# Optimization experiments

Hardware: AMD Instinct MI355X
Metric: run time of the kernel (lower is better)

The kernel has to match this reference:

```python
import jax, jax.numpy as jnp
import numpy as np


def setup_inputs() -> dict:
    key = jax.random.key(0)
    k1, k2 = jax.random.split(key)
    h = jax.random.normal(k1, (8, 16, 64, 512), dtype=jnp.float32)
    M = jax.random.normal(k2, (20000, 512), dtype=jnp.float32)
    return {"h": h, "M": M}


def reference(h, M):
    # h: [B, T, X, R], M: [K, R]
    B, T, X, R = h.shape
    hf = h.reshape(-1, R)                      # [N, R]
    att = jax.nn.softmax(hf @ M.T, axis=1)     # [N, K], unscaled dot-product
    out = att @ M                              # [N, R]
    return out.reshape(B, T, X, R)
```

## Files before the change

kernel.cpp:

```cpp
#include <hip/hip_runtime.h>
#include <stdint.h>

#define NQ 8192
#define NK 20000
#define RD 512
#define NT 157
#define TS0 79

typedef float f32x4 __attribute__((ext_vector_type(4)));
typedef short s16x8 __attribute__((ext_vector_type(8)));

__device__ __forceinline__ unsigned short bf16_rn(float x) {
    uint32_t u = __float_as_uint(x);
    return (unsigned short)((u + 0x7FFFu + ((u >> 16) & 1)) >> 16);
}

__device__ __forceinline__ void lds_barrier() {
    asm volatile("s_waitcnt lgkmcnt(0)\n\ts_barrier" ::: "memory");
}

__global__ void preconv_kernel(const float* __restrict__ M,
                               unsigned short* __restrict__ Mhi,
                               unsigned short* __restrict__ Mlo,
                               unsigned short* __restrict__ MT) {
    __shared__ float tilef[64 * 65];
    const int k0 = blockIdx.x * 64, r0 = blockIdx.y * 64;
    const int t = threadIdx.x;
#pragma unroll
    for (int i = 0; i < 16; i++) {
        int e = t + i * 256;
        int kr = e >> 6, cc = e & 63;
        int key = k0 + kr;
        if (key < NK) {
            float x = M[(size_t)key * RD + r0 + cc];
            uint32_t u = __float_as_uint(x);
            Mhi[(size_t)key * RD + r0 + cc] = (unsigned short)(u >> 16);
            Mlo[(size_t)key * RD + r0 + cc] = bf16_rn(x - __uint_as_float(u & 0xFFFF0000u));
            tilef[cc * 65 + kr] = x;
        }
    }
    __syncthreads();
#pragma unroll
    for (int i = 0; i < 16; i++) {
        int e = t + i * 256;
        int rr = e >> 6, kk = e & 63;
        int key = k0 + kk;
        if (key < NK) MT[(size_t)(r0 + rr) * NK + key] = bf16_rn(tilef[rr * 65 + kk]);
    }
}

__global__ __launch_bounds__(256, 2) void flash6_kernel(
        const float* __restrict__ h,
        const unsigned short* __restrict__ Mhi,
        const unsigned short* __restrict__ Mlo,
        const unsigned short* __restrict__ MT,
        float* __restrict__ out,
        float* __restrict__ Opart,
        float* __restrict__ mpart,
        float* __restrict__ lpart,
        int nsplit) {
    __shared__ unsigned short qbuf[32768];
    __shared__ unsigned short pbuf[8 * 512];
    __shared__ float smaxb[4 * 2 * 16];
    __shared__ float ssumb[4 * 2 * 16];

    const int tid = threadIdx.x;
    const int ch = tid >> 6, l = tid & 63;
    const int l15 = l & 15, q4 = l >> 4;
    const int kq = (l15 >> 3) & 1, jj = l15 & 7;

    int qb, split;
    if (nsplit == 2) { split = blockIdx.x & 1; qb = blockIdx.x >> 1; }
    else             { split = 0;              qb = blockIdx.x; }
    const int koff = (split == 0) ? 0 : TS0 * 128;
    const int ntl  = (nsplit == 2) ? ((split == 0) ? TS0 : (NT - TS0)) : NT;
    const int total_ks = ntl * 16;
    const int qbase = qb * 32;

    const size_t base_w = (size_t)(ch * 32 + l15) * RD + q4 * 8;
    auto kaddr = [&](int g, int cb) -> size_t {
        if (g >= total_ks) g = total_ks - 1;
        int t2 = g >> 4, s2 = g & 15;
        return (size_t)(koff + t2 * 128) * RD + (size_t)s2 * 32 + base_w + (size_t)cb * (16 * RD);
    };

    s16x8 kh[2][4], kl[2][4];
#pragma unroll
    for (int i = 0; i < 4; i++) {
        size_t a0 = kaddr(i, 0), a1 = kaddr(i, 1);
        kh[0][i] = *(const s16x8*)(Mhi + a0);
        kl[0][i] = *(const s16x8*)(Mlo + a0);
        kh[1][i] = *(const s16x8*)(Mhi + a1);
        kl[1][i] = *(const s16x8*)(Mlo + a1);
    }

#pragma unroll
    for (int i = 0; i < 8; i++) {
        int g = tid + i * 256;
        int row = g >> 6, s = (g >> 2) & 15, qg = g & 3;
        int strip = row >> 4, lrow = row & 15;
        const float* src = h + (size_t)(qbase + row) * RD + s * 32 + qg * 8;
        f32x4 a = *(const f32x4*)src;
        f32x4 b = *(const f32x4*)(src + 4);
        s16x8 hi8, lo8;
#pragma unroll
        for (int j = 0; j < 8; j++) {
            float x = (j < 4) ? a[j] : b[j - 4];
            uint32_t u = __float_as_uint(x);
            hi8[j] = (short)(u >> 16);
            lo8[j] = (short)bf16_rn(x - __uint_as_float(u & 0xFFFF0000u));
        }
        int off = ((strip * 16 + s) * 512 + (qg * 16 + lrow) * 8);
        *(s16x8*)&qbuf[off] = hi8;
        *(s16x8*)&qbuf[16384 + off] = lo8;
    }
    lds_barrier();

    f32x4 O[2][8];
#pragma unroll
    for (int st = 0; st < 2; st++)
#pragma unroll
        for (int ct = 0; ct < 8; ct++) O[st][ct] = 0.f;
    f32x4 m_run[2], l_run[2];
    m_run[0] = -3e38f; m_run[1] = -3e38f; l_run[0] = 0.f; l_run[1] = 0.f;

    for (int tile = 0; tile < ntl; tile++) {
        f32x4 C[2][2];
        C[0][0] = 0.f; C[0][1] = 0.f; C[1][0] = 0.f; C[1][1] = 0.f;
#pragma unroll
        for (int s = 0; s < 16; s++) {
            const int sl = s & 3;
            s16x8 kh0 = kh[0][sl], kl0 = kl[0][sl];
            s16x8 kh1 = kh[1][sl], kl1 = kl[1][sl];
            {
                int g = tile * 16 + s + 4;
                size_t a0 = kaddr(g, 0), a1 = kaddr(g, 1);
                kh[0][sl] = *(const s16x8*)(Mhi + a0);
                kl[0][sl] = *(const s16x8*)(Mlo + a0);
                kh[1][sl] = *(const s16x8*)(Mhi + a1);
                kl[1][sl] = *(const s16x8*)(Mlo + a1);
            }
#pragma unroll
            for (int st = 0; st < 2; st++) {
                s16x8 qh = *(const s16x8*)&qbuf[(st * 16 + s) * 512 + l * 8];
                s16x8 ql = *(const s16x8*)&qbuf[16384 + (st * 16 + s) * 512 + l * 8];
                C[st][0] = __builtin_amdgcn_mfma_f32_16x16x32_bf16(qh, kh0, C[st][0], 0, 0, 0);
                C[st][1] = __builtin_amdgcn_mfma_f32_16x16x32_bf16(qh, kh1, C[st][1], 0, 0, 0);
                C[st][0] = __builtin_amdgcn_mfma_f32_16x16x32_bf16(ql, kh0, C[st][0], 0, 0, 0);
                C[st][1] = __builtin_amdgcn_mfma_f32_16x16x32_bf16(ql, kh1, C[st][1], 0, 0, 0);
                C[st][0] = __builtin_amdgcn_mfma_f32_16x16x32_bf16(qh, kl0, C[st][0], 0, 0, 0);
                C[st][1] = __builtin_amdgcn_mfma_f32_16x16x32_bf16(qh, kl1, C[st][1], 0, 0, 0);
            }
        }
        if (tile == ntl - 1) {
#pragma unroll
            for (int cb = 0; cb < 2; cb++) {
                int kg = koff + tile * 128 + ch * 32 + cb * 16 + l15;
                if (kg >= NK) { C[0][cb] = -3e38f; C[1][cb] = -3e38f; }
            }
        }

        const unsigned short* mtp = MT + (size_t)(ch * 128 + l15) * NK + koff + tile * 128 + q4 * 8;
        s16x8 bt[2][4];
#pragma unroll
        for (int sk = 0; sk < 4; sk++) {
            bt[0][sk] = *(const s16x8*)(mtp + sk * 32);
            bt[1][sk] = *(const s16x8*)(mtp + (size_t)16 * NK + sk * 32);
        }

        f32x4 mx[2];
#pragma unroll
        for (int st = 0; st < 2; st++)
#pragma unroll
            for (int v = 0; v < 4; v++) mx[st][v] = fmaxf(C[st][0][v], C[st][1][v]);
#pragma unroll
        for (int d = 1; d < 16; d <<= 1) {
#pragma unroll
            for (int st = 0; st < 2; st++)
#pragma unroll
                for (int v = 0; v < 4; v++) mx[st][v] = fmaxf(mx[st][v], __shfl_xor(mx[st][v], d, 16));
        }
        if (l15 == 0) {
            *(f32x4*)&smaxb[(ch * 2 + 0) * 16 + q4 * 4] = mx[0];
            *(f32x4*)&smaxb[(ch * 2 + 1) * 16 + q4 * 4] = mx[1];
        }
        lds_barrier();
        f32x4 mnew[2]; mnew[0] = m_run[0]; mnew[1] = m_run[1];
#pragma unroll
        for (int cc = 0; cc < 4; cc++) {
#pragma unroll
            for (int st = 0; st < 2; st++) {
                f32x4 tv = *(const f32x4*)&smaxb[(cc * 2 + st) * 16 + q4 * 4];
#pragma unroll
                for (int v = 0; v < 4; v++) mnew[st][v] = fmaxf(mnew[st][v], tv[v]);
            }
        }
        f32x4 alpha[2];
#pragma unroll
        for (int st = 0; st < 2; st++)
#pragma unroll
            for (int v = 0; v < 4; v++) {
                alpha[st][v] = __expf(m_run[st][v] - mnew[st][v]);
                m_run[st][v] = mnew[st][v];
            }
        f32x4 ps[2]; ps[0] = 0.f; ps[1] = 0.f;
#pragma unroll
        for (int st = 0; st < 2; st++) {
#pragma unroll
            for (int cb = 0; cb < 2; cb++) {
#pragma unroll
                for (int v = 0; v < 4; v++) {
                    float p = __expf(C[st][cb][v] - mnew[st][v]);
                    ps[st][v] += p;
                    pbuf[(ch * 2 + st) * 512 + ((cb * 2 + kq) * 16 + q4 * 4 + v) * 8 + jj] = bf16_rn(p);
                }
            }
        }
#pragma unroll
        for (int d = 1; d < 16; d <<= 1) {
#pragma unroll
            for (int st = 0; st < 2; st++)
#pragma unroll
                for (int v = 0; v < 4; v++) ps[st][v] += __shfl_xor(ps[st][v], d, 16);
        }
        if (l15 == 0) {
            *(f32x4*)&ssumb[(ch * 2 + 0) * 16 + q4 * 4] = ps[0];
            *(f32x4*)&ssumb[(ch * 2 + 1) * 16 + q4 * 4] = ps[1];
        }
        lds_barrier();
        f32x4 ts[2]; ts[0] = 0.f; ts[1] = 0.f;
#pragma unroll
        for (int cc = 0; cc < 4; cc++) {
            ts[0] += *(const f32x4*)&ssumb[(cc * 2 + 0) * 16 + q4 * 4];
            ts[1] += *(const f32x4*)&ssumb[(cc * 2 + 1) * 16 + q4 * 4];
        }
#pragma unroll
        for (int st = 0; st < 2; st++)
#pragma unroll
            for (int v = 0; v < 4; v++) l_run[st][v] = l_run[st][v] * alpha[st][v] + ts[st][v];
#pragma unroll
        for (int st = 0; st < 2; st++)
#pragma unroll
            for (int ct = 0; ct < 8; ct++)
#pragma unroll
                for (int v = 0; v < 4; v++) O[st][ct][v] *= alpha[st][v];
        s16x8 pa[2][4];
#pragma unroll
        for (int st = 0; st < 2; st++)
#pragma unroll
            for (int sk = 0; sk < 4; sk++)
                pa[st][sk] = *(const s16x8*)&pbuf[((sk * 2 + st) * 512) + l * 8];

#pragma unroll
        for (int ct = 0; ct < 8; ct++) {
            s16x8 b0 = bt[ct & 1][0], b1 = bt[ct & 1][1], b2 = bt[ct & 1][2], b3 = bt[ct & 1][3];
            if (ct < 6) {
#pragma unroll
                for (int sk = 0; sk < 4; sk++)
                    bt[ct & 1][sk] = *(const s16x8*)(mtp + (size_t)(ct + 2) * 16 * NK + sk * 32);
            }
            O[0][ct] = __builtin_amdgcn_mfma_f32_16x16x32_bf16(pa[0][0], b0, O[0][ct], 0, 0, 0);
            O[1][ct] = __builtin_amdgcn_mfma_f32_16x16x32_bf16(pa[1][0], b0, O[1][ct], 0, 0, 0);
            O[0][ct] = __builtin_amdgcn_mfma_f32_16x16x32_bf16(pa[0][1], b1, O[0][ct], 0, 0, 0);
            O[1][ct] = __builtin_amdgcn_mfma_f32_16x16x32_bf16(pa[1][1], b1, O[1][ct], 0, 0, 0);
            O[0][ct] = __builtin_amdgcn_mfma_f32_16x16x32_bf16(pa[0][2], b2, O[0][ct], 0, 0, 0);
            O[1][ct] = __builtin_amdgcn_mfma_f32_16x16x32_bf16(pa[1][2], b2, O[1][ct], 0, 0, 0);
            O[0][ct] = __builtin_amdgcn_mfma_f32_16x16x32_bf16(pa[0][3], b3, O[0][ct], 0, 0, 0);
            O[1][ct] = __builtin_amdgcn_mfma_f32_16x16x32_bf16(pa[1][3], b3, O[1][ct], 0, 0, 0);
        }
        lds_barrier();
    }

    if (nsplit == 2) {
        float* Od = Opart + (size_t)split * NQ * RD;
#pragma unroll
        for (int st = 0; st < 2; st++)
#pragma unroll
            for (int ct = 0; ct < 8; ct++)
#pragma unroll
                for (int v = 0; v < 4; v++)
                    Od[(size_t)(qbase + st * 16 + q4 * 4 + v) * RD + ch * 128 + ct * 16 + l15] =
                        O[st][ct][v];
        if (ch == 0 && l15 == 0) {
#pragma unroll
            for (int st = 0; st < 2; st++)
#pragma unroll
                for (int v = 0; v < 4; v++) {
                    mpart[split * NQ + qbase + st * 16 + q4 * 4 + v] = m_run[st][v];
                    lpart[split * NQ + qbase + st * 16 + q4 * 4 + v] = l_run[st][v];
                }
        }
    } else {
#pragma unroll
        for (int st = 0; st < 2; st++)
#pragma unroll
            for (int ct = 0; ct < 8; ct++)
#pragma unroll
                for (int v = 0; v < 4; v++)
                    out[(size_t)(qbase + st * 16 + q4 * 4 + v) * RD + ch * 128 + ct * 16 + l15] =
                        O[st][ct][v] / l_run[st][v];
    }
}

__global__ __launch_bounds__(256) void combine_kernel(const float* __restrict__ Opart,
                                                      const float* __restrict__ mpart,
                                                      const float* __restrict__ lpart,
                                                      float* __restrict__ out) {
    const int t = threadIdx.x;
    const int row = blockIdx.x * 2 + (t >> 7);
    const int d = (t & 127) * 4;
    float m0 = mpart[row], m1 = mpart[NQ + row];
    float l0 = lpart[row], l1 = lpart[NQ + row];
    float m = fmaxf(m0, m1);
    float w0 = __expf(m0 - m), w1 = __expf(m1 - m);
    float inv = 1.f / (w0 * l0 + w1 * l1);
    f32x4 o0 = *(const f32x4*)&Opart[(size_t)row * RD + d];
    f32x4 o1 = *(const f32x4*)&Opart[(size_t)NQ * RD + (size_t)row * RD + d];
    f32x4 r;
#pragma unroll
    for (int v = 0; v < 4; v++) r[v] = (o0[v] * w0 + o1[v] * w1) * inv;
    *(f32x4*)&out[(size_t)row * RD + d] = r;
}

__global__ __launch_bounds__(256) void naive_kernel(const float* __restrict__ h,
                                                    const float* __restrict__ M,
                                                    float* __restrict__ out) {
    __shared__ float hs[16 * 520];
    __shared__ float ms[8 * 520];
    __shared__ float sdot[2][128];
    __shared__ float sm[16], sl[16], sal[16], sp[16][8];
    const int t = threadIdx.x;
    const int qbase = blockIdx.x * 16;
#pragma unroll
    for (int i = 0; i < 32; i++) {
        int e = t + i * 256;
        int row = e >> 9, col = e & 511;
        hs[row * 520 + col] = h[(size_t)(qbase + row) * RD + col];
    }
    if (t < 16) { sm[t] = -3e38f; sl[t] = 0.f; }
    float Oacc[32];
#pragma unroll
    for (int i = 0; i < 32; i++) Oacc[i] = 0.f;
    const int q = t >> 4;
    const int eb = (t & 15) * 32;

    for (int k0 = 0; k0 < NK; k0 += 8) {
        __syncthreads();
#pragma unroll
        for (int i = 0; i < 16; i++) {
            int e = t + i * 256;
            if (e < 4096) {
                int kk = e >> 9, col = e & 511;
                ms[kk * 520 + col] = M[(size_t)(k0 + kk) * RD + col];
            }
        }
        __syncthreads();
        {
            int pair = t & 127, half = t >> 7;
            int qq = pair & 15, kk = pair >> 4;
            const float* hp = &hs[qq * 520 + half * 256];
            const float* mp = &ms[kk * 520 + half * 256];
            float acc = 0.f;
#pragma unroll 8
            for (int e = 0; e < 256; e++) acc += hp[e] * mp[e];
            sdot[half][pair] = acc;
        }
        __syncthreads();
        if (t < 16) {
            int qq = t;
            float s8[8];
#pragma unroll
            for (int kk = 0; kk < 8; kk++) s8[kk] = sdot[0][qq + 16 * kk] + sdot[1][qq + 16 * kk];
            float mn = sm[qq];
#pragma unroll
            for (int kk = 0; kk < 8; kk++) mn = fmaxf(mn, s8[kk]);
            float al = __expf(sm[qq] - mn);
            float addl = 0.f;
#pragma unroll
            for (int kk = 0; kk < 8; kk++) { float p = __expf(s8[kk] - mn); sp[qq][kk] = p; addl += p; }
            sm[qq] = mn; sl[qq] = sl[qq] * al + addl; sal[qq] = al;
        }
        __syncthreads();
        {
            float al = sal[q];
#pragma unroll
            for (int i = 0; i < 32; i++) Oacc[i] *= al;
#pragma unroll
            for (int kk = 0; kk < 8; kk++) {
                float p = sp[q][kk];
                const float* mp = &ms[kk * 520 + eb];
#pragma unroll
                for (int i = 0; i < 32; i++) Oacc[i] += p * mp[i];
            }
        }
    }
    __syncthreads();
    float inv = 1.f / sl[q];
#pragma unroll
    for (int i = 0; i < 32; i++) out[(size_t)(qbase + q) * RD + eb + i] = Oacc[i] * inv;
}

extern "C" void kernel_launch(void* const* d_in, const int* in_sizes, int n_in,
                              void* d_out, int out_size, void* d_ws, size_t ws_size,
                              hipStream_t stream) {
    const float* h = (const float*)d_in[0];
    const float* M = (const float*)d_in[1];
    float* out = (float*)d_out;
    const size_t seg = (size_t)NK * RD;
    const size_t base_bytes = (seg * 3ull + 8192ull) * 2ull;
    const size_t opart_bytes = 2ull * NQ * RD * 4ull;
    const size_t stat_bytes = 2ull * 2ull * NQ * 4ull;
    const size_t need_split = base_bytes + opart_bytes + stat_bytes;

    if (ws_size >= base_bytes) {
        unsigned short* Mhi = (unsigned short*)d_ws;
        unsigned short* Mlo = Mhi + seg;
        unsigned short* MT  = Mlo + seg;
        float* Opart = (float*)((char*)d_ws + base_bytes);
        float* mpart = Opart + 2ull * NQ * RD;
        float* lpart = mpart + 2ull * NQ;
        preconv_kernel<<<dim3(313, 8), 256, 0, stream>>>(M, Mhi, Mlo, MT);
        if (ws_size >= need_split) {
            flash6_kernel<<<512, 256, 0, stream>>>(h, Mhi, Mlo, MT, out, Opart, mpart, lpart, 2);
            combine_kernel<<<NQ / 2, 256, 0, stream>>>(Opart, mpart, lpart, out);
        } else {
            flash6_kernel<<<256, 256, 0, stream>>>(h, Mhi, Mlo, MT, out, Opart, mpart, lpart, 1);
        }
    } else {
        naive_kernel<<<512, 256, 0, stream>>>(h, M, out);
    }
}
```

Baseline: 1.593 ms.

## Software-pipeline QK^T of next tile with softmax and PV of previous tile

Restructures the main loop so the QK^T MFMA steps for tile i are split into chunks and interleaved around the barriers of the softmax/PV phase for tile i-1. The last tile is handled in an epilogue after the loop, and the trailing per-iteration barrier is dropped. The aim is to hide barrier waits, exp work and LDS latency behind matrix work. Keeping two score tiles live raises register pressure, which could cause spills.

```diff
diff --git a/kernel.cpp b/kernel.cpp
--- a/kernel.cpp
+++ b/kernel.cpp
@@ -49,7 +49,32 @@
     }
 }
 
-__global__ __launch_bounds__(256, 2) void flash6_kernel(
+#define S_STEP(ii, s_) do {                                                                        \
+        const int sl_ = (s_) & 3;                                                                  \
+        s16x8 kh0_ = kh[0][sl_], kl0_ = kl[0][sl_];                                                \
+        s16x8 kh1_ = kh[1][sl_], kl1_ = kl[1][sl_];                                                \
+        {                                                                                          \
+            int g_ = (ii) * 16 + (s_) + 4;                                                         \
+            size_t a0_ = kaddr(g_, 0), a1_ = kaddr(g_, 1);                                         \
+            kh[0][sl_] = *(const s16x8*)(Mhi + a0_);                                               \
+            kl[0][sl_] = *(const s16x8*)(Mlo + a0_);                                               \
+            kh[1][sl_] = *(const s16x8*)(Mhi + a1_);                                               \
+            kl[1][sl_] = *(const s16x8*)(Mlo + a1_);                                               \
+        }                                                                                          \
+        _Pragma("unroll")                                                                          \
+        for (int st_ = 0; st_ < 2; st_++) {                                                        \
+            s16x8 qh_ = *(const s16x8*)&qbuf[(st_ * 16 + (s_)) * 512 + l * 8];                     \
+            s16x8 ql_ = *(const s16x8*)&qbuf[16384 + (st_ * 16 + (s_)) * 512 + l * 8];             \
+            Cc[st_][0] = __builtin_amdgcn_mfma_f32_16x16x32_bf16(qh_, kh0_, Cc[st_][0], 0, 0, 0);  \
+            Cc[st_][1] = __builtin_amdgcn_mfma_f32_16x16x32_bf16(qh_, kh1_, Cc[st_][1], 0, 0, 0);  \
+            Cc[st_][0] = __builtin_amdgcn_mfma_f32_16x16x32_bf16(ql_, kh0_, Cc[st_][0], 0, 0, 0);  \
+            Cc[st_][1] = __builtin_amdgcn_mfma_f32_16x16x32_bf16(ql_, kh1_, Cc[st_][1], 0, 0, 0);  \
+            Cc[st_][0] = __builtin_amdgcn_mfma_f32_16x16x32_bf16(qh_, kl0_, Cc[st_][0], 0, 0, 0);  \
+            Cc[st_][1] = __builtin_amdgcn_mfma_f32_16x16x32_bf16(qh_, kl1_, Cc[st_][1], 0, 0, 0);  \
+        }                                                                                          \
+    } while (0)
+
+__global__ __launch_bounds__(256, 2) void flash7_kernel(
         const float* __restrict__ h,
         const unsigned short* __restrict__ Mhi,
         const unsigned short* __restrict__ Mlo,
@@ -124,55 +149,33 @@
     f32x4 m_run[2], l_run[2];
     m_run[0] = -3e38f; m_run[1] = -3e38f; l_run[0] = 0.f; l_run[1] = 0.f;
 
-    for (int tile = 0; tile < ntl; tile++) {
-        f32x4 C[2][2];
-        C[0][0] = 0.f; C[0][1] = 0.f; C[1][0] = 0.f; C[1][1] = 0.f;
-#pragma unroll
-        for (int s = 0; s < 16; s++) {
-            const int sl = s & 3;
-            s16x8 kh0 = kh[0][sl], kl0 = kl[0][sl];
-            s16x8 kh1 = kh[1][sl], kl1 = kl[1][sl];
-            {
-                int g = tile * 16 + s + 4;
-                size_t a0 = kaddr(g, 0), a1 = kaddr(g, 1);
-                kh[0][sl] = *(const s16x8*)(Mhi + a0);
-                kl[0][sl] = *(const s16x8*)(Mlo + a0);
-                kh[1][sl] = *(const s16x8*)(Mhi + a1);
-                kl[1][sl] = *(const s16x8*)(Mlo + a1);
-            }
-#pragma unroll
-            for (int st = 0; st < 2; st++) {
-                s16x8 qh = *(const s16x8*)&qbuf[(st * 16 + s) * 512 + l * 8];
-                s16x8 ql = *(const s16x8*)&qbuf[16384 + (st * 16 + s) * 512 + l * 8];
-                C[st][0] = __builtin_amdgcn_mfma_f32_16x16x32_bf16(qh, kh0, C[st][0], 0, 0, 0);
-                C[st][1] = __builtin_amdgcn_mfma_f32_16x16x32_bf16(qh, kh1, C[st][1], 0, 0, 0);
-                C[st][0] = __builtin_amdgcn_mfma_f32_16x16x32_bf16(ql, kh0, C[st][0], 0, 0, 0);
-                C[st][1] = __builtin_amdgcn_mfma_f32_16x16x32_bf16(ql, kh1, C[st][1], 0, 0, 0);
-                C[st][0] = __builtin_amdgcn_mfma_f32_16x16x32_bf16(qh, kl0, C[st][0], 0, 0, 0);
-                C[st][1] = __builtin_amdgcn_mfma_f32_16x16x32_bf16(qh, kl1, C[st][1], 0, 0, 0);
-            }
-        }
-        if (tile == ntl - 1) {
-#pragma unroll
-            for (int cb = 0; cb < 2; cb++) {
-                int kg = koff + tile * 128 + ch * 32 + cb * 16 + l15;
-                if (kg >= NK) { C[0][cb] = -3e38f; C[1][cb] = -3e38f; }
-            }
-        }
-
-        const unsigned short* mtp = MT + (size_t)(ch * 128 + l15) * NK + koff + tile * 128 + q4 * 8;
+    f32x4 Cc[2][2];
+    Cc[0][0] = 0.f; Cc[0][1] = 0.f; Cc[1][0] = 0.f; Cc[1][1] = 0.f;
+#pragma unroll
+    for (int s = 0; s < 16; s++) S_STEP(0, s);
+
+    for (int i = 1; i < ntl; i++) {
+        const int prv = i - 1;
+
+        f32x4 Cp[2][2];
+#pragma unroll
+        for (int st = 0; st < 2; st++) {
+            Cp[st][0] = Cc[st][0]; Cp[st][1] = Cc[st][1];
+            Cc[st][0] = 0.f;       Cc[st][1] = 0.f;
+        }
+
+        const unsigned short* mtp = MT + (size_t)(ch * 128 + l15) * NK + koff + prv * 128 + q4 * 8;
         s16x8 bt[2][4];
 #pragma unroll
         for (int sk = 0; sk < 4; sk++) {
             bt[0][sk] = *(const s16x8*)(mtp + sk * 32);
             bt[1][sk] = *(const s16x8*)(mtp + (size_t)16 * NK + sk * 32);
         }
-
         f32x4 mx[2];
 #pragma unroll
         for (int st = 0; st < 2; st++)
 #pragma unroll
-            for (int v = 0; v < 4; v++) mx[st][v] = fmaxf(C[st][0][v], C[st][1][v]);
+            for (int v = 0; v < 4; v++) mx[st][v] = fmaxf(Cp[st][0][v], Cp[st][1][v]);
 #pragma unroll
         for (int d = 1; d < 16; d <<= 1) {
 #pragma unroll
@@ -184,7 +187,10 @@
             *(f32x4*)&smaxb[(ch * 2 + 0) * 16 + q4 * 4] = mx[0];
             *(f32x4*)&smaxb[(ch * 2 + 1) * 16 + q4 * 4] = mx[1];
         }
+#pragma unroll
+        for (int s = 0; s < 5; s++) S_STEP(i, s);
         lds_barrier();
+
         f32x4 mnew[2]; mnew[0] = m_run[0]; mnew[1] = m_run[1];
 #pragma unroll
         for (int cc = 0; cc < 4; cc++) {
@@ -210,7 +216,7 @@
             for (int cb = 0; cb < 2; cb++) {
 #pragma unroll
                 for (int v = 0; v < 4; v++) {
-                    float p = __expf(C[st][cb][v] - mnew[st][v]);
+                    float p = __expf(Cp[st][cb][v] - mnew[st][v]);
                     ps[st][v] += p;
                     pbuf[(ch * 2 + st) * 512 + ((cb * 2 + kq) * 16 + q4 * 4 + v) * 8 + jj] = bf16_rn(p);
                 }
@@ -227,7 +233,10 @@
             *(f32x4*)&ssumb[(ch * 2 + 0) * 16 + q4 * 4] = ps[0];
             *(f32x4*)&ssumb[(ch * 2 + 1) * 16 + q4 * 4] = ps[1];
         }
+#pragma unroll
+        for (int s = 5; s < 11; s++) S_STEP(i, s);
         lds_barrier();
+
         f32x4 ts[2]; ts[0] = 0.f; ts[1] = 0.f;
 #pragma unroll
         for (int cc = 0; cc < 4; cc++) {
@@ -250,7 +259,8 @@
 #pragma unroll
             for (int sk = 0; sk < 4; sk++)
                 pa[st][sk] = *(const s16x8*)&pbuf[((sk * 2 + st) * 512) + l * 8];
-
+#pragma unroll
+        for (int s = 11; s < 16; s++) S_STEP(i, s);
 #pragma unroll
         for (int ct = 0; ct < 8; ct++) {
             s16x8 b0 = bt[ct & 1][0], b1 = bt[ct & 1][1], b2 = bt[ct & 1][2], b3 = bt[ct & 1][3];
@@ -268,7 +278,121 @@
             O[0][ct] = __builtin_amdgcn_mfma_f32_16x16x32_bf16(pa[0][3], b3, O[0][ct], 0, 0, 0);
             O[1][ct] = __builtin_amdgcn_mfma_f32_16x16x32_bf16(pa[1][3], b3, O[1][ct], 0, 0, 0);
         }
+    }
+
+    {
+        const int prv = ntl - 1;
+#pragma unroll
+        for (int cb = 0; cb < 2; cb++) {
+            int kg = koff + prv * 128 + ch * 32 + cb * 16 + l15;
+            if (kg >= NK) { Cc[0][cb] = -3e38f; Cc[1][cb] = -3e38f; }
+        }
+        const unsigned short* mtp = MT + (size_t)(ch * 128 + l15) * NK + koff + prv * 128 + q4 * 8;
+        s16x8 bt[2][4];
+#pragma unroll
+        for (int sk = 0; sk < 4; sk++) {
+            bt[0][sk] = *(const s16x8*)(mtp + sk * 32);
+            bt[1][sk] = *(const s16x8*)(mtp + (size_t)16 * NK + sk * 32);
+        }
+        f32x4 mx[2];
+#pragma unroll
+        for (int st = 0; st < 2; st++)
+#pragma unroll
+            for (int v = 0; v < 4; v++) mx[st][v] = fmaxf(Cc[st][0][v], Cc[st][1][v]);
+#pragma unroll
+        for (int d = 1; d < 16; d <<= 1) {
+#pragma unroll
+            for (int st = 0; st < 2; st++)
+#pragma unroll
+                for (int v = 0; v < 4; v++) mx[st][v] = fmaxf(mx[st][v], __shfl_xor(mx[st][v], d, 16));
+        }
+        if (l15 == 0) {
+            *(f32x4*)&smaxb[(ch * 2 + 0) * 16 + q4 * 4] = mx[0];
+            *(f32x4*)&smaxb[(ch * 2 + 1) * 16 + q4 * 4] = mx[1];
+        }
         lds_barrier();
+        f32x4 mnew[2]; mnew[0] = m_run[0]; mnew[1] = m_run[1];
+#pragma unroll
+        for (int cc = 0; cc < 4; cc++) {
+#pragma unroll
+            for (int st = 0; st < 2; st++) {
+                f32x4 tv = *(const f32x4*)&smaxb[(cc * 2 + st) * 16 + q4 * 4];
+#pragma unroll
+                for (int v = 0; v < 4; v++) mnew[st][v] = fmaxf(mnew[st][v], tv[v]);
+            }
+        }
+        f32x4 alpha[2];
+#pragma unroll
+        for (int st = 0; st < 2; st++)
+#pragma unroll
+            for (int v = 0; v < 4; v++) {
+                alpha[st][v] = __expf(m_run[st][v] - mnew[st][v]);
+                m_run[st][v] = mnew[st][v];
+            }
+        f32x4 ps[2]; ps[0] = 0.f; ps[1] = 0.f;
+#pragma unroll
+        for (int st = 0; st < 2; st++) {
+#pragma unroll
+            for (int cb = 0; cb < 2; cb++) {
+#pragma unroll
+                for (int v = 0; v < 4; v++) {
+                    float p = __expf(Cc[st][cb][v] - mnew[st][v]);
+                    ps[st][v] += p;
+                    pbuf[(ch * 2 + st) * 512 + ((cb * 2 + kq) * 16 + q4 * 4 + v) * 8 + jj] = bf16_rn(p);
+                }
+            }
+        }
+#pragma unroll
+        for (int d = 1; d < 16; d <<= 1) {
+#pragma unroll
+            for (int st = 0; st < 2; st++)
+#pragma unroll
+                for (int v = 0; v < 4; v++) ps[st][v] += __shfl_xor(ps[st][v], d, 16);
+        }
+        if (l15 == 0) {
+            *(f32x4*)&ssumb[(ch * 2 + 0) * 16 + q4 * 4] = ps[0];
+            *(f32x4*)&ssumb[(ch * 2 + 1) * 16 + q4 * 4] = ps[1];
+        }
+        lds_barrier();
+        f32x4 ts[2]; ts[0] = 0.f; ts[1] = 0.f;
+#pragma unroll
+        for (int cc = 0; cc < 4; cc++) {
+            ts[0] += *(const f32x4*)&ssumb[(cc * 2 + 0) * 16 + q4 * 4];
+            ts[1] += *(const f32x4*)&ssumb[(cc * 2 + 1) * 16 + q4 * 4];
+        }
+#pragma unroll
+        for (int st = 0; st < 2; st++)
+#pragma unroll
+            for (int v = 0; v < 4; v++) l_run[st][v] = l_run[st][v] * alpha[st][v] + ts[st][v];
+#pragma unroll
+        for (int st = 0; st < 2; st++)
+#pragma unroll
+            for (int ct = 0; ct < 8; ct++)
+#pragma unroll
+                for (int v = 0; v < 4; v++) O[st][ct][v] *= alpha[st][v];
+        s16x8 pa[2][4];
+#pragma unroll
+        for (int st = 0; st < 2; st++)
+#pragma unroll
+            for (int sk = 0; sk < 4; sk++)
+                pa[st][sk] = *(const s16x8*)&pbuf[((sk * 2 + st) * 512) + l * 8];
+#pragma unroll
+        for (int ct = 0; ct < 8; ct++) {
+            s16x8 b0 = bt[ct & 1][0], b1 = bt[ct & 1][1], b2 = bt[ct & 1][2], b3 = bt[ct & 1][3];
+            if (ct < 6) {
+#pragma unroll
+                for (int sk = 0; sk < 4; sk++)
+                    bt[ct & 1][sk] = *(const s16x8*)(mtp + (size_t)(ct + 2) * 16 * NK + sk * 32);
+            }
+            O[0][ct] = __builtin_amdgcn_mfma_f32_16x16x32_bf16(pa[0][0], b0, O[0][ct], 0, 0, 0);
+            O[1][ct] = __builtin_amdgcn_mfma_f32_16x16x32_bf16(pa[1][0], b0, O[1][ct], 0, 0, 0);
+            O[0][ct] = __builtin_amdgcn_mfma_f32_16x16x32_bf16(pa[0][1], b1, O[0][ct], 0, 0, 0);
+            O[1][ct] = __builtin_amdgcn_mfma_f32_16x16x32_bf16(pa[1][1], b1, O[1][ct], 0, 0, 0);
+            O[0][ct] = __builtin_amdgcn_mfma_f32_16x16x32_bf16(pa[0][2], b2, O[0][ct], 0, 0, 0);
+            O[1][ct] = __builtin_amdgcn_mfma_f32_16x16x32_bf16(pa[1][2], b2, O[1][ct], 0, 0, 0);
+            O[0][ct] = __builtin_amdgcn_mfma_f32_16x16x32_bf16(pa[0][3], b3, O[0][ct], 0, 0, 0);
+            O[1][ct] = __builtin_amdgcn_mfma_f32_16x16x32_bf16(pa[1][3], b3, O[1][ct], 0, 0, 0);
+        }
     }
 
     if (nsplit == 2) {
@@ -421,10 +545,10 @@
         float* lpart = mpart + 2ull * NQ;
         preconv_kernel<<<dim3(313, 8), 256, 0, stream>>>(M, Mhi, Mlo, MT);
         if (ws_size >= need_split) {
-            flash6_kernel<<<512, 256, 0, stream>>>(h, Mhi, Mlo, MT, out, Opart, mpart, lpart, 2);
+            flash7_kernel<<<512, 256, 0, stream>>>(h, Mhi, Mlo, MT, out, Opart, mpart, lpart, 2);
             combine_kernel<<<NQ / 2, 256, 0, stream>>>(Opart, mpart, lpart, out);
         } else {
-            flash6_kernel<<<256, 256, 0, stream>>>(h, Mhi, Mlo, MT, out, Opart, mpart, lpart, 1);
+            flash7_kernel<<<256, 256, 0, stream>>>(h, Mhi, Mlo, MT, out, Opart, mpart, lpart, 1);
         }
     } else {
         naive_kernel<<<512, 256, 0, stream>>>(h, M, out);
```

Measured after the change: 1.586 ms. About the same (-0.4%).

## Halve query tile, raise occupancy, software-pipeline QK^T of next tile with softmax/PV

Applied to the files above, without the earlier changes.

Each block now handles 16 query rows instead of 32, which halves LDS and register footprint and doubles the grid, and launch bounds are raised to 4 blocks per CU. The main loop is software-pipelined: the QK^T MFMA steps for tile i are interleaved between the barriers, max/sum reductions and PV accumulation of tile i-1, with a drained epilogue for the last tile. The aim is to hide barrier and softmax latency and raise occupancy. The trade-off is that each key tile (Mhi/Mlo/MT) is now reloaded by twice as many blocks, which increases memory and L2 traffic, and the prefetch depth drops to 2.

```diff
diff --git a/kernel.cpp b/kernel.cpp
--- a/kernel.cpp
+++ b/kernel.cpp
@@ -49,7 +49,29 @@
     }
 }
 
-__global__ __launch_bounds__(256, 2) void flash6_kernel(
+#define S_STEP(ii, s_) do {                                                                        \
+        const int sl_ = (s_) & 1;                                                                  \
+        s16x8 kh0_ = kh[0][sl_], kl0_ = kl[0][sl_];                                                \
+        s16x8 kh1_ = kh[1][sl_], kl1_ = kl[1][sl_];                                                \
+        {                                                                                          \
+            int g_ = (ii) * 16 + (s_) + 2;                                                         \
+            size_t a0_ = kaddr(g_, 0), a1_ = kaddr(g_, 1);                                         \
+            kh[0][sl_] = *(const s16x8*)(Mhi + a0_);                                               \
+            kl[0][sl_] = *(const s16x8*)(Mlo + a0_);                                               \
+            kh[1][sl_] = *(const s16x8*)(Mhi + a1_);                                               \
+            kl[1][sl_] = *(const s16x8*)(Mlo + a1_);                                               \
+        }                                                                                          \
+        s16x8 qh_ = *(const s16x8*)&qbuf[(s_) * 512 + l * 8];                                      \
+        s16x8 ql_ = *(const s16x8*)&qbuf[8192 + (s_) * 512 + l * 8];                               \
+        Cc[0] = __builtin_amdgcn_mfma_f32_16x16x32_bf16(qh_, kh0_, Cc[0], 0, 0, 0);                \
+        Cc[1] = __builtin_amdgcn_mfma_f32_16x16x32_bf16(qh_, kh1_, Cc[1], 0, 0, 0);                \
+        Cc[0] = __builtin_amdgcn_mfma_f32_16x16x32_bf16(ql_, kh0_, Cc[0], 0, 0, 0);                \
+        Cc[1] = __builtin_amdgcn_mfma_f32_16x16x32_bf16(ql_, kh1_, Cc[1], 0, 0, 0);                \
+        Cc[0] = __builtin_amdgcn_mfma_f32_16x16x32_bf16(qh_, kl0_, Cc[0], 0, 0, 0);                \
+        Cc[1] = __builtin_amdgcn_mfma_f32_16x16x32_bf16(qh_, kl1_, Cc[1], 0, 0, 0);                \
+    } while (0)
+
+__global__ __launch_bounds__(256, 4) void flash11_kernel(
         const float* __restrict__ h,
         const unsigned short* __restrict__ Mhi,
         const unsigned short* __restrict__ Mlo,
@@ -59,10 +81,10 @@
         float* __restrict__ mpart,
         float* __restrict__ lpart,
         int nsplit) {
-    __shared__ unsigned short qbuf[32768];
-    __shared__ unsigned short pbuf[8 * 512];
-    __shared__ float smaxb[4 * 2 * 16];
-    __shared__ float ssumb[4 * 2 * 16];
+    __shared__ unsigned short qbuf[16384];
+    __shared__ unsigned short pbuf[4 * 512];
+    __shared__ float smaxb[4 * 16];
+    __shared__ float ssumb[4 * 16];
 
     const int tid = threadIdx.x;
     const int ch = tid >> 6, l = tid & 63;
@@ -75,7 +97,7 @@
     const int koff = (split == 0) ? 0 : TS0 * 128;
     const int ntl  = (nsplit == 2) ? ((split == 0) ? TS0 : (NT - TS0)) : NT;
     const int total_ks = ntl * 16;
-    const int qbase = qb * 32;
+    const int qbase = qb * 16;
 
     const size_t base_w = (size_t)(ch * 32 + l15) * RD + q4 * 8;
     auto kaddr = [&](int g, int cb) -> size_t {
@@ -84,9 +106,9 @@
         return (size_t)(koff + t2 * 128) * RD + (size_t)s2 * 32 + base_w + (size_t)cb * (16 * RD);
     };
 
-    s16x8 kh[2][4], kl[2][4];
-#pragma unroll
-    for (int i = 0; i < 4; i++) {
+    s16x8 kh[2][2], kl[2][2];
+#pragma unroll
+    for (int i = 0; i < 2; i++) {
         size_t a0 = kaddr(i, 0), a1 = kaddr(i, 1);
         kh[0][i] = *(const s16x8*)(Mhi + a0);
         kl[0][i] = *(const s16x8*)(Mlo + a0);
@@ -95,10 +117,9 @@
     }
 
 #pragma unroll
-    for (int i = 0; i < 8; i++) {
+    for (int i = 0; i < 4; i++) {
         int g = tid + i * 256;
         int row = g >> 6, s = (g >> 2) & 15, qg = g & 3;
-        int strip = row >> 4, lrow = row & 15;
         const float* src = h + (size_t)(qbase + row) * RD + s * 32 + qg * 8;
         f32x4 a = *(const f32x4*)src;
         f32x4 b = *(const f32x4*)(src + 4);
@@ -110,147 +131,94 @@
             hi8[j] = (short)(u >> 16);
             lo8[j] = (short)bf16_rn(x - __uint_as_float(u & 0xFFFF0000u));
         }
-        int off = ((strip * 16 + s) * 512 + (qg * 16 + lrow) * 8);
+        int off = (s * 512 + (qg * 16 + row) * 8);
         *(s16x8*)&qbuf[off] = hi8;
-        *(s16x8*)&qbuf[16384 + off] = lo8;
+        *(s16x8*)&qbuf[8192 + off] = lo8;
     }
     lds_barrier();
 
-    f32x4 O[2][8];
-#pragma unroll
-    for (int st = 0; st < 2; st++)
-#pragma unroll
-        for (int ct = 0; ct < 8; ct++) O[st][ct] = 0.f;
-    f32x4 m_run[2], l_run[2];
-    m_run[0] = -3e38f; m_run[1] = -3e38f; l_run[0] = 0.f; l_run[1] = 0.f;
-
-    for (int tile = 0; tile < ntl; tile++) {
-        f32x4 C[2][2];
-        C[0][0] = 0.f; C[0][1] = 0.f; C[1][0] = 0.f; C[1][1] = 0.f;
-#pragma unroll
-        for (int s = 0; s < 16; s++) {
-            const int sl = s & 3;
-            s16x8 kh0 = kh[0][sl], kl0 = kl[0][sl];
-            s16x8 kh1 = kh[1][sl], kl1 = kl[1][sl];
-            {
-                int g = tile * 16 + s + 4;
-                size_t a0 = kaddr(g, 0), a1 = kaddr(g, 1);
-                kh[0][sl] = *(const s16x8*)(Mhi + a0);
-                kl[0][sl] = *(const s16x8*)(Mlo + a0);
-                kh[1][sl] = *(const s16x8*)(Mhi + a1);
-                kl[1][sl] = *(const s16x8*)(Mlo + a1);
-            }
-#pragma unroll
-            for (int st = 0; st < 2; st++) {
-                s16x8 qh = *(const s16x8*)&qbuf[(st * 16 + s) * 512 + l * 8];
-                s16x8 ql = *(const s16x8*)&qbuf[16384 + (st * 16 + s) * 512 + l * 8];
-                C[st][0] = __builtin_amdgcn_mfma_f32_16x16x32_bf16(qh, kh0, C[st][0], 0, 0, 0);
-                C[st][1] = __builtin_amdgcn_mfma_f32_16x16x32_bf16(qh, kh1, C[st][1], 0, 0, 0);
-                C[st][0] = __builtin_amdgcn_mfma_f32_16x16x32_bf16(ql, kh0, C[st][0], 0, 0, 0);
-                C[st][1] = __builtin_amdgcn_mfma_f32_16x16x32_bf16(ql, kh1, C[st][1], 0, 0, 0);
-                C[st][0] = __builtin_amdgcn_mfma_f32_16x16x32_bf16(qh, kl0, C[st][0], 0, 0, 0);
-                C[st][1] = __builtin_amdgcn_mfma_f32_16x16x32_bf16(qh, kl1, C[st][1], 0, 0, 0);
-            }
-        }
-        if (tile == ntl - 1) {
-#pragma unroll
-            for (int cb = 0; cb < 2; cb++) {
-                int kg = koff + tile * 128 + ch * 32 + cb * 16 + l15;
-                if (kg >= NK) { C[0][cb] = -3e38f; C[1][cb] = -3e38f; }
-            }
-        }
-
-        const unsigned short* mtp = MT + (size_t)(ch * 128 + l15) * NK + koff + tile * 128 + q4 * 8;
+    f32x4 O[8];
+#pragma unroll
+    for (int ct = 0; ct < 8; ct++) O[ct] = 0.f;
+    f32x4 m_run = -3e38f, l_run = 0.f;
+
+    f32x4 Cc[2];
+    Cc[0] = 0.f; Cc[1] = 0.f;
+#pragma unroll
+    for (int s = 0; s < 16; s++) S_STEP(0, s);
+
+    for (int i = 1; i < ntl; i++) {
+        const int prv = i - 1;
+
+        f32x4 Cp[2];
+        Cp[0] = Cc[0]; Cp[1] = Cc[1];
+        Cc[0] = 0.f;   Cc[1] = 0.f;
+
+        f32x4 mx;
+#pragma unroll
+        for (int v = 0; v < 4; v++) mx[v] = fmaxf(Cp[0][v], Cp[1][v]);
+#pragma unroll
+        for (int d = 1; d < 16; d <<= 1)
+#pragma unroll
+            for (int v = 0; v < 4; v++) mx[v] = fmaxf(mx[v], __shfl_xor(mx[v], d, 16));
+        if (l15 == 0) *(f32x4*)&smaxb[ch * 16 + q4 * 4] = mx;
+#pragma unroll
+        for (int s = 0; s < 6; s++) S_STEP(i, s);
+        lds_barrier();
+
+        f32x4 mnew = m_run;
+#pragma unroll
+        for (int cc = 0; cc < 4; cc++) {
+            f32x4 tv = *(const f32x4*)&smaxb[cc * 16 + q4 * 4];
+#pragma unroll
+            for (int v = 0; v < 4; v++) mnew[v] = fmaxf(mnew[v], tv[v]);
+        }
+        f32x4 alpha;
+#pragma unroll
+        for (int v = 0; v < 4; v++) {
+            alpha[v] = __expf(m_run[v] - mnew[v]);
+            m_run[v] = mnew[v];
+        }
+        f32x4 ps = 0.f;
+#pragma unroll
+        for (int cb = 0; cb < 2; cb++) {
+#pragma unroll
+            for (int v = 0; v < 4; v++) {
+                float p = __expf(Cp[cb][v] - mnew[v]);
+                ps[v] += p;
+                pbuf[ch * 512 + ((cb * 2 + kq) * 16 + q4 * 4 + v) * 8 + jj] = bf16_rn(p);
+            }
+        }
+#pragma unroll
+        for (int d = 1; d < 16; d <<= 1)
+#pragma unroll
+            for (int v = 0; v < 4; v++) ps[v] += __shfl_xor(ps[v], d, 16);
+        if (l15 == 0) *(f32x4*)&ssumb[ch * 16 + q4 * 4] = ps;
+#pragma unroll
+        for (int s = 6; s < 13; s++) S_STEP(i, s);
+        lds_barrier();
+
+        f32x4 ts = 0.f;
+#pragma unroll
+        for (int cc = 0; cc < 4; cc++) ts += *(const f32x4*)&ssumb[cc * 16 + q4 * 4];
+#pragma unroll
+        for (int v = 0; v < 4; v++) l_run[v] = l_run[v] * alpha[v] + ts[v];
+#pragma unroll
+        for (int ct = 0; ct < 8; ct++)
+#pragma unroll
+            for (int v = 0; v < 4; v++) O[ct][v] *= alpha[v];
+        s16x8 pa[4];
+#pragma unroll
+        for (int sk = 0; sk < 4; sk++) pa[sk] = *(const s16x8*)&pbuf[sk * 512 + l * 8];
+        const unsigned short* mtp = MT + (size_t)(ch * 128 + l15) * NK + koff + prv * 128 + q4 * 8;
         s16x8 bt[2][4];
 #pragma unroll
         for (int sk = 0; sk < 4; sk++) {
             bt[0][sk] = *(const s16x8*)(mtp + sk * 32);
             bt[1][sk] = *(const s16x8*)(mtp + (size_t)16 * NK + sk * 32);
         }
-
-        f32x4 mx[2];
-#pragma unroll
-        for (int st = 0; st < 2; st++)
-#pragma unroll
-            for (int v = 0; v < 4; v++) mx[st][v] = fmaxf(C[st][0][v], C[st][1][v]);
-#pragma unroll
-        for (int d = 1; d < 16; d <<= 1) {
-#pragma unroll
-            for (int st = 0; st < 2; st++)
-#pragma unroll
-                for (int v = 0; v < 4; v++) mx[st][v] = fmaxf(mx[st][v], __shfl_xor(mx[st][v], d, 16));
-        }
-        if (l15 == 0) {
-            *(f32x4*)&smaxb[(ch * 2 + 0) * 16 + q4 * 4] = mx[0];
-            *(f32x4*)&smaxb[(ch * 2 + 1) * 16 + q4 * 4] = mx[1];
-        }
-        lds_barrier();
-        f32x4 mnew[2]; mnew[0] = m_run[0]; mnew[1] = m_run[1];
-#pragma unroll
-        for (int cc = 0; cc < 4; cc++) {
-#pragma unroll
-            for (int st = 0; st < 2; st++) {
-                f32x4 tv = *(const f32x4*)&smaxb[(cc * 2 + st) * 16 + q4 * 4];
-#pragma unroll
-                for (int v = 0; v < 4; v++) mnew[st][v] = fmaxf(mnew[st][v], tv[v]);
-            }
-        }
-        f32x4 alpha[2];
-#pragma unroll
-        for (int st = 0; st < 2; st++)
-#pragma unroll
-            for (int v = 0; v < 4; v++) {
-                alpha[st][v] = __expf(m_run[st][v] - mnew[st][v]);
-                m_run[st][v] = mnew[st][v];
-            }
-        f32x4 ps[2]; ps[0] = 0.f; ps[1] = 0.f;
-#pragma unroll
-        for (int st = 0; st < 2; st++) {
-#pragma unroll
-            for (int cb = 0; cb < 2; cb++) {
-#pragma unroll
-                for (int v = 0; v < 4; v++) {
-                    float p = __expf(C[st][cb][v] - mnew[st][v]);
-                    ps[st][v] += p;
-                    pbuf[(ch * 2 + st) * 512 + ((cb * 2 + kq) * 16 + q4 * 4 + v) * 8 + jj] = bf16_rn(p);
-                }
-            }
-        }
-#pragma unroll
-        for (int d = 1; d < 16; d <<= 1) {
-#pragma unroll
-            for (int st = 0; st < 2; st++)
-#pragma unroll
-                for (int v = 0; v < 4; v++) ps[st][v] += __shfl_xor(ps[st][v], d, 16);
-        }
-        if (l15 == 0) {
-            *(f32x4*)&ssumb[(ch * 2 + 0) * 16 + q4 * 4] = ps[0];
-            *(f32x4*)&ssumb[(ch * 2 + 1) * 16 + q4 * 4] = ps[1];
-        }
-        lds_barrier();
-        f32x4 ts[2]; ts[0] = 0.f; ts[1] = 0.f;
-#pragma unroll
-        for (int cc = 0; cc < 4; cc++) {
-            ts[0] += *(const f32x4*)&ssumb[(cc * 2 + 0) * 16 + q4 * 4];
-            ts[1] += *(const f32x4*)&ssumb[(cc * 2 + 1) * 16 + q4 * 4];
-        }
-#pragma unroll
-        for (int st = 0; st < 2; st++)
-#pragma unroll
-            for (int v = 0; v < 4; v++) l_run[st][v] = l_run[st][v] * alpha[st][v] + ts[st][v];
-#pragma unroll
-        for (int st = 0; st < 2; st++)
-#pragma unroll
-            for (int ct = 0; ct < 8; ct++)
-#pragma unroll
-                for (int v = 0; v < 4; v++) O[st][ct][v] *= alpha[st][v];
-        s16x8 pa[2][4];
-#pragma unroll
-        for (int st = 0; st < 2; st++)
-#pragma unroll
-            for (int sk = 0; sk < 4; sk++)
-                pa[st][sk] = *(const s16x8*)&pbuf[((sk * 2 + st) * 512) + l * 8];
-
+#pragma unroll
+        for (int s = 13; s < 16; s++) S_STEP(i, s);
 #pragma unroll
         for (int ct = 0; ct < 8; ct++) {
             s16x8 b0 = bt[ct & 1][0], b1 = bt[ct & 1][1], b2 = bt[ct & 1][2], b3 = bt[ct & 1][3];
@@ -259,46 +227,113 @@
                 for (int sk = 0; sk < 4; sk++)
                     bt[ct & 1][sk] = *(const s16x8*)(mtp + (size_t)(ct + 2) * 16 * NK + sk * 32);
             }
-            O[0][ct] = __builtin_amdgcn_mfma_f32_16x16x32_bf16(pa[0][0], b0, O[0][ct], 0, 0, 0);
-            O[1][ct] = __builtin_amdgcn_mfma_f32_16x16x32_bf16(pa[1][0], b0, O[1][ct], 0, 0, 0);
-            O[0][ct] = __builtin_amdgcn_mfma_f32_16x16x32_bf16(pa[0][1], b1, O[0][ct], 0, 0, 0);
-            O[1][ct] = __builtin_amdgcn_mfma_f32_16x16x32_bf16(pa[1][1], b1, O[1][ct], 0, 0, 0);
-            O[0][ct] = __builtin_amdgcn_mfma_f32_16x16x32_bf16(pa[0][2], b2, O[0][ct], 0, 0, 0);
-            O[1][ct] = __builtin_amdgcn_mfma_f32_16x16x32_bf16(pa[1][2], b2, O[1][ct], 0, 0, 0);
-            O[0][ct] = __builtin_amdgcn_mfma_f32_16x16x32_bf16(pa[0][3], b3, O[0][ct], 0, 0, 0);
-            O[1][ct] = __builtin_amdgcn_mfma_f32_16x16x32_bf16(pa[1][3], b3, O[1][ct], 0, 0, 0);
-        }
+            O[ct] = __builtin_amdgcn_mfma_f32_16x16x32_bf16(pa[0], b0, O[ct], 0, 0, 0);
+            O[ct] = __builtin_amdgcn_mfma_f32_16x16x32_bf16(pa[1], b1, O[ct], 0, 0, 0);
+            O[ct] = __builtin_amdgcn_mfma_f32_16x16x32_bf16(pa[2], b2, O[ct], 0, 0, 0);
+            O[ct] = __builtin_amdgcn_mfma_f32_16x16x32_bf16(pa[3], b3, O[ct], 0, 0, 0);
+        }
+    }
+
+    {
+        const int prv = ntl - 1;
+#pragma unroll
+        for (int cb = 0; cb < 2; cb++) {
+            int kg = koff + prv * 128 + ch * 32 + cb * 16 + l15;
+            if (kg >= NK) Cc[cb] = -3e38f;
+        }
+        f32x4 mx;
+#pragma unroll
+        for (int v = 0; v < 4; v++) mx[v] = fmaxf(Cc[0][v], Cc[1][v]);
+#pragma unroll
+        for (int d = 1; d < 16; d <<= 1)
+#pragma unroll
+            for (int v = 0; v < 4; v++) mx[v] = fmaxf(mx[v], __shfl_xor(mx[v], d, 16));
+        if (l15 == 0) *(f32x4*)&smaxb[ch * 16 + q4 * 4] = mx;
         lds_barrier();
+        f32x4 mnew = m_run;
+#pragma unroll
+        for (int cc = 0; cc < 4; cc++) {
+            f32x4 tv = *(const f32x4*)&smaxb[cc * 16 + q4 * 4];
+#pragma unroll
+            for (int v = 0; v < 4; v++) mnew[v] = fmaxf(mnew[v], tv[v]);
+        }
+        f32x4 alpha;
+#pragma unroll
+        for (int v = 0; v < 4; v++) {
+            alpha[v] = __expf(m_run[v] - mnew[v]);
+            m_run[v] = mnew[v];
+        }
+        f32x4 ps = 0.f;
+#pragma unroll
+        for (int cb = 0; cb < 2; cb++) {
+#pragma unroll
+            for (int v = 0; v < 4; v++) {
+                float p = __expf(Cc[cb][v] - mnew[v]);
+                ps[v] += p;
+                pbuf[ch * 512 + ((cb * 2 + kq) * 16 + q4 * 4 + v) * 8 + jj] = bf16_rn(p);
+            }
+        }
+#pragma unroll
+        for (int d = 1; d < 16; d <<= 1)
+#pragma unroll
+            for (int v = 0; v < 4; v++) ps[v] += __shfl_xor(ps[v], d, 16);
+        if (l15 == 0) *(f32x4*)&ssumb[ch * 16 + q4 * 4] = ps;
+        lds_barrier();
+        f32x4 ts = 0.f;
+#pragma unroll
+        for (int cc = 0; cc < 4; cc++) ts += *(const f32x4*)&ssumb[cc * 16 + q4 * 4];
+#pragma unroll
+        for (int v = 0; v < 4; v++) l_run[v] = l_run[v] * alpha[v] + ts[v];
+#pragma unroll
+        for (int ct = 0; ct < 8; ct++)
+#pragma unroll
+            for (int v = 0; v < 4; v++) O[ct][v] *= alpha[v];
+        s16x8 pa[4];
+#pragma unroll
+        for (int sk = 0; sk < 4; sk++) pa[sk] = *(const s16x8*)&pbuf[sk * 512 + l * 8];
+        const unsigned short* mtp = MT + (size_t)(ch * 128 + l15) * NK + koff + prv * 128 + q4 * 8;
+        s16x8 bt[2][4];
+#pragma unroll
+        for (int sk = 0; sk < 4; sk++) {
+            bt[0][sk] = *(const s16x8*)(mtp + sk * 32);
+            bt[1][sk] = *(const s16x8*)(mtp + (size_t)16 * NK + sk * 32);
+        }
+#pragma unroll
+        for (int ct = 0; ct < 8; ct++) {
+            s16x8 b0 = bt[ct & 1][0], b1 = bt[ct & 1][1], b2 = bt[ct & 1][2], b3 = bt[ct & 1][3];
+            if (ct < 6) {
+#pragma unroll
+                for (int sk = 0; sk < 4; sk++)
+                    bt[ct & 1][sk] = *(const s16x8*)(mtp + (size_t)(ct + 2) * 16 * NK + sk * 32);
+            }
+            O[ct] = __builtin_amdgcn_mfma_f32_16x16x32_bf16(pa[0], b0, O[ct], 0, 0, 0);
+            O[ct] = __builtin_amdgcn_mfma_f32_16x16x32_bf16(pa[1], b1, O[ct], 0, 0, 0);
+            O[ct] = __builtin_amdgcn_mfma_f32_16x16x32_bf16(pa[2], b2, O[ct], 0, 0, 0);
+            O[ct] = __builtin_amdgcn_mfma_f32_16x16x32_bf16(pa[3], b3, O[ct], 0, 0, 0);
+        }
     }
 
     if (nsplit == 2) {
         float* Od = Opart + (size_t)split * NQ * RD;
 #pragma unroll
-        for (int st = 0; st < 2; st++)
-#pragma unroll
-            for (int ct = 0; ct < 8; ct++)
-#pragma unroll
-                for (int v = 0; v < 4; v++)
-                    Od[(size_t)(qbase + st * 16 + q4 * 4 + v) * RD + ch * 128 + ct * 16 + l15] =
-                        O[st][ct][v];
+        for (int ct = 0; ct < 8; ct++)
+#pragma unroll
+            for (int v = 0; v < 4; v++)
+                Od[(size_t)(qbase + q4 * 4 + v) * RD + ch * 128 + ct * 16 + l15] = O[ct][v];
         if (ch == 0 && l15 == 0) {
 #pragma unroll
-            for (int st = 0; st < 2; st++)
-#pragma unroll
-                for (int v = 0; v < 4; v++) {
-                    mpart[split * NQ + qbase + st * 16 + q4 * 4 + v] = m_run[st][v];
-                    lpart[split * NQ + qbase + st * 16 + q4 * 4 + v] = l_run[st][v];
-                }
+            for (int v = 0; v < 4; v++) {
+                mpart[split * NQ + qbase + q4 * 4 + v] = m_run[v];
+                lpart[split * NQ + qbase + q4 * 4 + v] = l_run[v];
+            }
         }
     } else {
 #pragma unroll
-        for (int st = 0; st < 2; st++)
-#pragma unroll
-            for (int ct = 0; ct < 8; ct++)
-#pragma unroll
-                for (int v = 0; v < 4; v++)
-                    out[(size_t)(qbase + st * 16 + q4 * 4 + v) * RD + ch * 128 + ct * 16 + l15] =
-                        O[st][ct][v] / l_run[st][v];
+        for (int ct = 0; ct < 8; ct++)
+#pragma unroll
+            for (int v = 0; v < 4; v++)
+                out[(size_t)(qbase + q4 * 4 + v) * RD + ch * 128 + ct * 16 + l15] =
+                    O[ct][v] / l_run[v];
     }
 }
 
@@ -421,10 +456,10 @@
         float* lpart = mpart + 2ull * NQ;
         preconv_kernel<<<dim3(313, 8), 256, 0, stream>>>(M, Mhi, Mlo, MT);
         if (ws_size >= need_split) {
-            flash6_kernel<<<512, 256, 0, stream>>>(h, Mhi, Mlo, MT, out, Opart, mpart, lpart, 2);
+            flash11_kernel<<<1024, 256, 0, stream>>>(h, Mhi, Mlo, MT, out, Opart, mpart, lpart, 2);
             combine_kernel<<<NQ / 2, 256, 0, stream>>>(Opart, mpart, lpart, out);
         } else {
-            flash6_kernel<<<256, 256, 0, stream>>>(h, Mhi, Mlo, MT, out, Opart, mpart, lpart, 1);
+            flash11_kernel<<<512, 256, 0, stream>>>(h, Mhi, Mlo, MT, out, Opart, mpart, lpart, 1);
         }
     } else {
         naive_kernel<<<512, 256, 0, stream>>>(h, M, out);
```

Result: slower. 3.602 ms (+126.1%).
